# Kernel optimization log

Measured on AMD Instinct MI355X. Metric: run time of the kernel, lower is better.

Reference implementation:

```python
import jax, jax.numpy as jnp
import numpy as np

EPS = 1e-6
NHEAD = 12

def _ln(x):
    m = jnp.mean(x, -1, keepdims=True)
    v = jnp.var(x, -1, keepdims=True)
    return (x - m) * jax.lax.rsqrt(v + EPS)

def _modulate(x, shift, scale):
    return x * (1 + scale[:, None, :]) + shift[:, None, :]

def _pos_embedding(idx, dim, max_len=2048):
    K = jnp.arange(dim // 2)
    ang = idx[..., None] * jnp.pi / (max_len ** (2.0 * K / dim))
    return jnp.concatenate([jnp.sin(ang), jnp.cos(ang)], axis=-1)

def _forward(x, W_xemb, b_xemb, ds_table, sg_table, Wqkv, bqkv, Wo, bo, W1, b1, W2, b2,
             Wada, bada, Wada_f, bada_f, W_out, dataset, spacegroup, mask):
    B, N, _ = x.shape
    D = W_xemb.shape[1]
    hd = D // NHEAD
    # conditioning vector: label embeddings (eval mode: no cfg dropout)
    c = ds_table[dataset] + sg_table[spacegroup]                 # [B, D]
    h = x @ W_xemb + b_xemb + _pos_embedding(jnp.arange(N), D)[None]  # [B, N, D]
    kmask = mask[:, None, None, :]                                # [B,1,1,N], True = padded key
    scale_qk = 1.0 / jnp.sqrt(jnp.asarray(hd, h.dtype))

    def block(h, p):
        Wqkv, bqkv, Wo, bo, W1, b1, W2, b2, Wada, bada = p
        mods = jax.nn.silu(c) @ Wada + bada                      # [B, 6D]
        sh_a, sc_a, g_a, sh_m, sc_m, g_m = jnp.split(mods, 6, axis=-1)
        xm = _modulate(_ln(h), sh_a, sc_a)
        qkv = (xm @ Wqkv + bqkv).reshape(B, N, 3, NHEAD, hd)
        q, k, v = qkv[:, :, 0], qkv[:, :, 1], qkv[:, :, 2]
        scores = jnp.einsum('bqhd,bkhd->bhqk', q, k) * scale_qk   # MATH-backend path: full [B,H,N,N]
        scores = jnp.where(kmask, -jnp.inf, scores)
        attn = jax.nn.softmax(scores, axis=-1)
        o = jnp.einsum('bhqk,bkhd->bqhd', attn, v).reshape(B, N, D)
        o = o @ Wo + bo
        h = h + g_a[:, None, :] * o
        y = _modulate(_ln(h), sh_m, sc_m)
        y = jax.nn.gelu(y @ W1 + b1, approximate=True) @ W2 + b2
        h = h + g_m[:, None, :] * y
        return h, None

    h, _ = jax.lax.scan(block, h, (Wqkv, bqkv, Wo, bo, W1, b1, W2, b2, Wada, bada))
    mods_f = jax.nn.silu(c) @ Wada_f + bada_f
    sh_f, sc_f = jnp.split(mods_f, 2, axis=-1)
    return _modulate(_ln(h), sh_f, sc_f) @ W_out                  # [B, N, 1] per-token energy


def setup_inputs() -> dict:
    B, N, D, L, DX, HID = 32, 512, 768, 12, 8, 3072
    keys = iter(jax.random.split(jax.random.key(0), 32))
    def w(shape, s=0.02):
        return jax.random.normal(next(keys), shape, jnp.float32) * s
    return dict(
        x=jax.random.normal(next(keys), (B, N, 2 * DX), jnp.float32),
        W_xemb=w((2 * DX, D)), b_xemb=jnp.zeros((D,), jnp.float32),
        ds_table=w((3, D)), sg_table=w((231, D)),
        Wqkv=w((L, D, 3 * D)), bqkv=jnp.zeros((L, 3 * D), jnp.float32),
        Wo=w((L, D, D)), bo=jnp.zeros((L, D), jnp.float32),
        W1=w((L, D, HID)), b1=jnp.zeros((L, HID), jnp.float32),
        W2=w((L, HID, D)), b2=jnp.zeros((L, D), jnp.float32),
        Wada=w((L, D, 6 * D)), bada=jnp.zeros((L, 6 * D), jnp.float32),
        Wada_f=w((D, 2 * D)), bada_f=jnp.zeros((2 * D,), jnp.float32),
        W_out=w((D, 1)),
        dataset=jax.random.randint(next(keys), (32,), 0, 2),
        spacegroup=jax.random.randint(next(keys), (32,), 0, 230),
        mask=jax.random.bernoulli(next(keys), 0.1, (32, 512)),
    )


def reference(x, W_xemb, b_xemb, ds_table, sg_table, Wqkv, bqkv, Wo, bo, W1, b1, W2, b2,
              Wada, bada, Wada_f, bada_f, W_out, dataset, spacegroup, mask):
    return _forward(x, W_xemb, b_xemb, ds_table, sg_table, Wqkv, bqkv, Wo, bo, W1, b1,
                    W2, b2, Wada, bada, Wada_f, bada_f, W_out, dataset, spacegroup, mask)
```

## Files before the change

kernel.cpp:

```cpp
#include <hip/hip_runtime.h>
#include <hip/hip_bf16.h>

#define B_   32
#define N_   512
#define D_   768
#define H_   12
#define HID_ 3072
#define L_   12
#define M_   (B_*N_)

typedef __attribute__((ext_vector_type(8))) short short8_t;
typedef __attribute__((ext_vector_type(4))) short short4_t;
typedef __attribute__((ext_vector_type(4))) float f32x4;
typedef __hip_bfloat16 bf16;

__device__ __forceinline__ void gll16(const void* g, void* l){
    __builtin_amdgcn_global_load_lds((const __attribute__((address_space(1))) void*)g,
                                     (__attribute__((address_space(3))) void*)l, 16, 0, 0);
}

__global__ __launch_bounds__(256) void embed_kernel(
    const float* __restrict__ x, const float* __restrict__ Wx,
    const float* __restrict__ bx, float* __restrict__ h)
{
    long idx = (long)blockIdx.x * 256 + threadIdx.x;
    int d = (int)(idx % 768);
    long m = idx / 768;
    int n = (int)(m % 512);
    float acc = bx[d];
    const float* xr = x + m * 16;
    #pragma unroll
    for (int k = 0; k < 16; ++k) acc = fmaf(xr[k], Wx[k*768 + d], acc);
    int K = (d < 384) ? d : d - 384;
    float ang = (float)n * 3.14159265358979323846f * expf(-(2.0f*(float)K/768.0f) * 7.624618986159398f);
    acc += (d < 384) ? sinf(ang) : cosf(ang);
    h[idx] = acc;
}

__global__ __launch_bounds__(256) void csilu_kernel(
    const float* __restrict__ ds_t, const float* __restrict__ sg_t,
    const int* __restrict__ dataset, const int* __restrict__ sg, float* __restrict__ out)
{
    int idx = blockIdx.x*256 + threadIdx.x;
    int b = idx / 768, d = idx % 768;
    float c = ds_t[dataset[b]*768 + d] + sg_t[sg[b]*768 + d];
    out[idx] = c / (1.0f + expf(-c));
}

__global__ __launch_bounds__(256) void mods_part_kernel(
    const float* __restrict__ csilu, const float* __restrict__ W,
    float* __restrict__ part, int Nd2, long wLayerStride)
{
    __shared__ float cs[16][96];
    int n2 = blockIdx.x*256 + threadIdx.x;
    int l = blockIdx.y, z = blockIdx.z;
    int kz = z >> 1, bg = z & 1;
    int L = gridDim.y;
    for (int t = threadIdx.x; t < 16*96; t += 256){
        int bb = t / 96, kk = t - bb*96;
        cs[bb][kk] = csilu[(bg*16 + bb)*768 + kz*96 + kk];
    }
    __syncthreads();
    const float2* Wl = (const float2*)(W + (long)l*wLayerStride);
    float2 acc[16];
    #pragma unroll
    for (int b=0;b<16;b++) acc[b] = make_float2(0.f, 0.f);
    for (int k=0;k<96;++k){
        float2 wv = Wl[(long)(kz*96 + k)*Nd2 + n2];
        #pragma unroll
        for (int b=0;b<16;b++){
            float c = cs[b][k];
            acc[b].x = fmaf(c, wv.x, acc[b].x);
            acc[b].y = fmaf(c, wv.y, acc[b].y);
        }
    }
    float2* pp = (float2*)part + ((long)(kz*L + l)*32 + bg*16)*Nd2 + n2;
    #pragma unroll
    for (int b=0;b<16;b++) pp[(long)b*Nd2] = acc[b];
}

__global__ __launch_bounds__(256) void mods_reduce_kernel(
    const float* __restrict__ part, const float* __restrict__ bias,
    float* __restrict__ out, int Nd, int L)
{
    long idx = (long)blockIdx.x*256 + threadIdx.x;
    int n = (int)(idx % Nd);
    long r = idx / Nd;
    int b = (int)(r & 31);
    int l = (int)(r >> 5);
    float s = bias[(long)l*Nd + n];
    #pragma unroll
    for (int z=0;z<8;z++) s += part[((long)(z*L + l)*32 + b)*Nd + n];
    out[idx] = s;
}

__global__ __launch_bounds__(256) void transpose4_kernel(
    const float* __restrict__ Wqkv, const float* __restrict__ Wo,
    const float* __restrict__ W1,  const float* __restrict__ W2,
    bf16* __restrict__ wqT, bf16* __restrict__ woT,
    bf16* __restrict__ w1T, bf16* __restrict__ w2T)
{
    __shared__ float t[32][33];
    int tt = blockIdx.x;
    const float* src; bf16* dst; int K, Nd, nx;
    if (tt < 1728){ src=Wqkv; dst=wqT; K=768; Nd=2304; nx=72; }
    else if (tt < 2304){ src=Wo; dst=woT; K=768; Nd=768; nx=24; tt -= 1728; }
    else if (tt < 4608){ src=W1; dst=w1T; K=768; Nd=3072; nx=96; tt -= 2304; }
    else { src=W2; dst=w2T; K=3072; Nd=768; nx=24; tt -= 4608; }
    int n0 = (tt % nx)*32, k0 = (tt / nx)*32;
    int tx = threadIdx.x & 31, ty = threadIdx.x >> 5;
    #pragma unroll
    for (int j=0;j<4;j++)
        t[ty + j*8][tx] = src[(long)(k0 + ty + j*8)*Nd + n0 + tx];
    __syncthreads();
    #pragma unroll
    for (int j=0;j<4;j++)
        dst[(long)(n0 + ty + j*8)*K + k0 + tx] = __float2bfloat16(t[tx][ty + j*8]);
}

__global__ __launch_bounds__(256) void ln_mod_kernel(
    const float* __restrict__ h, const float* __restrict__ shiftB,
    const float* __restrict__ scaleB, int modsStride, bf16* __restrict__ out)
{
    int wave = threadIdx.x >> 6, lane = threadIdx.x & 63;
    long row = (long)blockIdx.x*4 + wave;
    int b = (int)(row >> 9);
    const float4* xr = (const float4*)(h + row*768);
    float4 v[3];
    float s = 0.f, ss = 0.f;
    #pragma unroll
    for (int i=0;i<3;i++){
        v[i] = xr[lane + i*64];
        s  += v[i].x + v[i].y + v[i].z + v[i].w;
        ss += v[i].x*v[i].x + v[i].y*v[i].y + v[i].z*v[i].z + v[i].w*v[i].w;
    }
    #pragma unroll
    for (int o=1;o<64;o<<=1){ s += __shfl_xor(s,o,64); ss += __shfl_xor(ss,o,64); }
    float mean = s * (1.0f/768.0f);
    float var  = ss * (1.0f/768.0f) - mean*mean;
    float rstd = rsqrtf(var + 1e-6f);
    const float4* sh4 = (const float4*)(shiftB + (long)b*modsStride);
    const float4* sc4 = (const float4*)(scaleB + (long)b*modsStride);
    short4_t* orow = (short4_t*)(out + row*768);
    #pragma unroll
    for (int i=0;i<3;i++){
        float4 sh = sh4[lane + i*64];
        float4 sc = sc4[lane + i*64];
        float o0 = (v[i].x-mean)*rstd*(1.f+sc.x) + sh.x;
        float o1 = (v[i].y-mean)*rstd*(1.f+sc.y) + sh.y;
        float o2 = (v[i].z-mean)*rstd*(1.f+sc.z) + sh.z;
        float o3 = (v[i].w-mean)*rstd*(1.f+sc.w) + sh.w;
        bf16 b0 = __float2bfloat16(o0), b1 = __float2bfloat16(o1);
        bf16 b2 = __float2bfloat16(o2), b3 = __float2bfloat16(o3);
        short4_t pk;
        pk[0] = *(short*)&b0; pk[1] = *(short*)&b1;
        pk[2] = *(short*)&b2; pk[3] = *(short*)&b3;
        orow[lane + i*64] = pk;
    }
}

__device__ __forceinline__ float gelu_f(float x){
    float z2 = 1.5957691216057308f * x * (1.0f + 0.044715f*x*x);
    return x / (1.0f + __expf(-z2));
}

template<int MODE>
__global__ __launch_bounds__(256, 2) void gemm128_kernel(
    const bf16* __restrict__ A, const bf16* __restrict__ Bw,
    const float* __restrict__ bias, bf16* __restrict__ outBf,
    float* __restrict__ hres, const float* __restrict__ gate,
    int Nd, int Kd, int gateStride)
{
    __shared__ __align__(16) short lds[40960];
    int tid = threadIdx.x;
    int lane = tid & 63, wave = tid >> 6;
    int frow = lane & 15, g = lane >> 4;

    int nx = gridDim.x;
    int bid = blockIdx.y * nx + blockIdx.x;
    int xcd = bid & 7;
    int wq  = bid >> 3;
    int mt  = xcd * 16 + (wq & 15);
    int ct  = wq >> 4;
    int m0 = mt * 128, n0 = ct * 192;
    int wn = wave * 48;

    const short* Ag = (const short*)A;
    const short* Bg = (const short*)Bw;
    int r0 = tid >> 3, s0 = (tid & 7) ^ ((tid >> 3) & 7);
    const short* aSrc = Ag + (long)(m0 + r0)*Kd + s0*8;
    const short* bSrc = Bg + (long)(n0 + r0)*Kd + s0*8;
    long rj = (long)32*Kd;
    int wbase = wave*512;

    int aFrag = frow*64;
    int bFrag = (wn + frow)*64;
    int slotK0 = (g ^ (frow & 7))*8;
    int slotK1 = ((4+g) ^ (frow & 7))*8;

    f32x4 acc[8][3];
    #pragma unroll
    for (int i=0;i<8;i++)
        #pragma unroll
        for (int j=0;j<3;j++) acc[i][j] = (f32x4){0.f,0.f,0.f,0.f};

    int NT = Kd >> 6;

#define STAGE(kt, ps) { \
    int par_ = (kt)&1; \
    if ((ps)==0){ \
        short* d_ = &lds[par_*8192 + wbase]; \
        gll16(aSrc +        (long)(kt)*64, d_); \
        gll16(aSrc +   rj + (long)(kt)*64, d_ + 2048); \
        gll16(aSrc + 2*rj + (long)(kt)*64, d_ + 4096); \
        gll16(aSrc + 3*rj + (long)(kt)*64, d_ + 6144); \
    } else { \
        short* d_ = &lds[16384 + par_*12288 + wbase]; \
        gll16(bSrc +        (long)(kt)*64, d_); \
        gll16(bSrc +   rj + (long)(kt)*64, d_ + 2048); \
        gll16(bSrc + 2*rj + (long)(kt)*64, d_ + 4096); \
        gll16(bSrc + 3*rj + (long)(kt)*64, d_ + 6144); \
        gll16(bSrc + 4*rj + (long)(kt)*64, d_ + 8192); \
        gll16(bSrc + 5*rj + (long)(kt)*64, d_ + 10240); \
    } }

    STAGE(0,0); STAGE(0,1);

    for (int kt=0; kt<NT; ++kt){
        int pA  = (kt&1)*8192;
        int pBb = 16384 + (kt&1)*12288;
        bool pf = (kt+1 < NT);
        if (pf){
            STAGE(kt+1, 0);
            asm volatile("s_waitcnt vmcnt(4)" ::: "memory");
        } else {
            asm volatile("s_waitcnt vmcnt(0)" ::: "memory");
        }
        __builtin_amdgcn_s_barrier();
        __builtin_amdgcn_sched_barrier(0);
        short8_t af[8], bfr[3];
        #pragma unroll
        for (int i=0;i<8;i++) af[i]  = *(const short8_t*)&lds[pA + aFrag + i*1024 + slotK0];
        #pragma unroll
        for (int j=0;j<3;j++) bfr[j] = *(const short8_t*)&lds[pBb + bFrag + j*1024 + slotK0];
        if (pf) STAGE(kt+1, 1);
        __builtin_amdgcn_s_setprio(1);
        #pragma unroll
        for (int i=0;i<8;i++)
            #pragma unroll
            for (int j=0;j<3;j++)
                acc[i][j] = __builtin_amdgcn_mfma_f32_16x16x32_bf16(af[i], bfr[j], acc[i][j], 0, 0, 0);
        __builtin_amdgcn_s_setprio(0);
        #pragma unroll
        for (int i=0;i<8;i++) af[i]  = *(const short8_t*)&lds[pA + aFrag + i*1024 + slotK1];
        #pragma unroll
        for (int j=0;j<3;j++) bfr[j] = *(const short8_t*)&lds[pBb + bFrag + j*1024 + slotK1];
        __builtin_amdgcn_s_setprio(1);
        #pragma unroll
        for (int i=0;i<8;i++)
            #pragma unroll
            for (int j=0;j<3;j++)
                acc[i][j] = __builtin_amdgcn_mfma_f32_16x16x32_bf16(af[i], bfr[j], acc[i][j], 0, 0, 0);
        __builtin_amdgcn_s_setprio(0);
        __builtin_amdgcn_sched_barrier(0);
        __builtin_amdgcn_s_barrier();
        __builtin_amdgcn_sched_barrier(0);
    }
#undef STAGE

    int rbase = m0 + g*4;
    int cbase = n0 + wn + frow;
    float bv0 = bias[cbase], bv1 = bias[cbase+16], bv2 = bias[cbase+32];
    #pragma unroll
    for (int i=0;i<8;i++){
        #pragma unroll
        for (int r=0;r<4;r++){
            int row = rbase + i*16 + r;
            float v0 = acc[i][0][r] + bv0;
            float v1 = acc[i][1][r] + bv1;
            float v2 = acc[i][2][r] + bv2;
            if (MODE == 0){
                bf16* o_ = outBf + (long)row*Nd + cbase;
                o_[0]  = __float2bfloat16(v0);
                o_[16] = __float2bfloat16(v1);
                o_[32] = __float2bfloat16(v2);
            } else if (MODE == 1){
                bf16* o_ = outBf + (long)row*Nd + cbase;
                o_[0]  = __float2bfloat16(gelu_f(v0));
                o_[16] = __float2bfloat16(gelu_f(v1));
                o_[32] = __float2bfloat16(gelu_f(v2));
            } else {
                int bb = row >> 9;
                const float* gp = gate + (long)bb*gateStride + cbase;
                float* hp = hres + (long)row*768 + cbase;
                hp[0]  += gp[0]  * v0;
                hp[16] += gp[16] * v1;
                hp[32] += gp[32] * v2;
            }
        }
    }
}

__global__ __launch_bounds__(256) void attn_mfma_kernel(
    const bf16* __restrict__ qkv, const int* __restrict__ mask, bf16* __restrict__ o)
{
    __shared__ __align__(16) short Ks[64][72];
    __shared__ __align__(16) short Vt[64][72];
    __shared__ __align__(16) short Ps[4][16][72];
    __shared__ float maskf[512];
    int tid = threadIdx.x, lane = tid & 63, wave = tid >> 6;
    int qt = blockIdx.x, hh = blockIdx.y, b = blockIdx.z;
    long base = (long)b * 512 * 2304;
    const short* qkvs = (const short*)qkv;

    maskf[tid]       = mask[b*512 + tid]       ? -1e30f : 0.0f;
    maskf[tid + 256] = mask[b*512 + tid + 256] ? -1e30f : 0.0f;

    int c = lane & 15, g = lane >> 4;
    int qrowA = qt*64 + wave*16 + c;
    const short* qptr = qkvs + base + (long)qrowA*2304 + hh*64 + g*8;
    short8_t qa0 = *(const short8_t*)qptr;
    short8_t qa1 = *(const short8_t*)(qptr + 32);

    f32x4 oacc[4];
    #pragma unroll
    for (int j=0;j<4;j++) oacc[j] = (f32x4){0.f,0.f,0.f,0.f};
    float m_r[4], l_r[4];
    #pragma unroll
    for (int r=0;r<4;r++){ m_r[r] = -50.0f; l_r[r] = 0.0f; }

    int kp = (tid & 31)*2, gv = tid >> 5;
    const short* kgbase = qkvs + base + 768  + hh*64;
    const short* vgbase = qkvs + base + 1536 + hh*64 + gv*8;

    for (int kt=0; kt<8; ++kt){
        __syncthreads();
        {
            int v0 = tid, v1 = tid + 256;
            int r0 = v0>>3, c0 = (v0&7)*8, r1 = v1>>3, c1 = (v1&7)*8;
            *(short8_t*)&Ks[r0][c0] = *(const short8_t*)(kgbase + (long)(kt*64 + r0)*2304 + c0);
            *(short8_t*)&Ks[r1][c1] = *(const short8_t*)(kgbase + (long)(kt*64 + r1)*2304 + c1);
            short8_t va = *(const short8_t*)(vgbase + (long)(kt*64 + kp    )*2304);
            short8_t vb = *(const short8_t*)(vgbase + (long)(kt*64 + kp + 1)*2304);
            #pragma unroll
            for (int e=0;e<8;e++){
                unsigned int pack = (unsigned int)(unsigned short)va[e]
                                  | ((unsigned int)(unsigned short)vb[e] << 16);
                *(unsigned int*)&Vt[gv*8 + e][kp] = pack;
            }
        }
        __syncthreads();
        f32x4 s[4];
        #pragma unroll
        for (int j=0;j<4;j++){
            short8_t kb0 = *(const short8_t*)&Ks[j*16 + c][g*8];
            short8_t kb1 = *(const short8_t*)&Ks[j*16 + c][g*8 + 32];
            f32x4 z = (f32x4){0.f,0.f,0.f,0.f};
            z = __builtin_amdgcn_mfma_f32_16x16x32_bf16(qa0, kb0, z, 0, 0, 0);
            z = __builtin_amdgcn_mfma_f32_16x16x32_bf16(qa1, kb1, z, 0, 0, 0);
            s[j] = z;
        }
        #pragma unroll
        for (int j=0;j<4;j++){
            float mbj = maskf[kt*64 + j*16 + c];
            #pragma unroll
            for (int r=0;r<4;r++) s[j][r] = s[j][r]*0.125f + mbj;
        }
        #pragma unroll
        for (int r=0;r<4;r++){
            float tm = fmaxf(fmaxf(s[0][r], s[1][r]), fmaxf(s[2][r], s[3][r]));
            #pragma unroll
            for (int o_=1;o_<16;o_<<=1) tm = fmaxf(tm, __shfl_xor(tm, o_, 64));
            float mn  = fmaxf(m_r[r], tm);
            float fac = __expf(m_r[r] - mn);
            m_r[r] = mn;
            float ls = l_r[r]*fac;
            #pragma unroll
            for (int j=0;j<4;j++){
                float p = __expf(s[j][r] - mn);
                s[j][r] = p;
                ls += p;
            }
            l_r[r] = ls;
            #pragma unroll
            for (int j=0;j<4;j++) oacc[j][r] *= fac;
        }
        #pragma unroll
        for (int j=0;j<4;j++)
            #pragma unroll
            for (int r=0;r<4;r++)
                *(bf16*)&Ps[wave][g*4 + r][j*16 + c] = __float2bfloat16(s[j][r]);
        short8_t pa0 = *(const short8_t*)&Ps[wave][c][g*8];
        short8_t pa1 = *(const short8_t*)&Ps[wave][c][g*8 + 32];
        #pragma unroll
        for (int j=0;j<4;j++){
            short8_t vb0 = *(const short8_t*)&Vt[j*16 + c][g*8];
            short8_t vb1 = *(const short8_t*)&Vt[j*16 + c][g*8 + 32];
            oacc[j] = __builtin_amdgcn_mfma_f32_16x16x32_bf16(pa0, vb0, oacc[j], 0, 0, 0);
            oacc[j] = __builtin_amdgcn_mfma_f32_16x16x32_bf16(pa1, vb1, oacc[j], 0, 0, 0);
        }
    }
    #pragma unroll
    for (int r=0;r<4;r++){
        float lt = l_r[r];
        #pragma unroll
        for (int o_=1;o_<16;o_<<=1) lt += __shfl_xor(lt, o_, 64);
        l_r[r] = 1.0f / lt;
    }
    int qrowC = qt*64 + wave*16 + g*4;
    bf16* orow = o + ((long)b*512 + qrowC)*768 + hh*64;
    #pragma unroll
    for (int r=0;r<4;r++)
        #pragma unroll
        for (int j=0;j<4;j++)
            orow[(long)r*768 + j*16 + c] = __float2bfloat16(oacc[j][r] * l_r[r]);
}

__global__ __launch_bounds__(256) void outdot_kernel(
    const bf16* __restrict__ xm, const float* __restrict__ Wout, float* __restrict__ out)
{
    int tid=threadIdx.x, lane=tid&63, wave=tid>>6;
    long row = (long)blockIdx.x*4 + wave;
    const bf16* xr = xm + row*768;
    float acc = 0.f;
    #pragma unroll
    for (int i=0;i<12;i++){ int d = lane + i*64; acc = fmaf(__bfloat162float(xr[d]), Wout[d], acc); }
    #pragma unroll
    for (int o_=1;o_<64;o_<<=1) acc += __shfl_xor(acc, o_, 64);
    if (lane==0) out[row] = acc;
}

extern "C" void kernel_launch(void* const* d_in, const int* in_sizes, int n_in,
                              void* d_out, int out_size, void* d_ws, size_t ws_size,
                              hipStream_t stream)
{
    const float* x      = (const float*)d_in[0];
    const float* W_xemb = (const float*)d_in[1];
    const float* b_xemb = (const float*)d_in[2];
    const float* ds_t   = (const float*)d_in[3];
    const float* sg_t   = (const float*)d_in[4];
    const float* Wqkv   = (const float*)d_in[5];
    const float* bqkv   = (const float*)d_in[6];
    const float* Wo     = (const float*)d_in[7];
    const float* bo     = (const float*)d_in[8];
    const float* W1     = (const float*)d_in[9];
    const float* b1     = (const float*)d_in[10];
    const float* W2     = (const float*)d_in[11];
    const float* b2     = (const float*)d_in[12];
    const float* Wada   = (const float*)d_in[13];
    const float* bada   = (const float*)d_in[14];
    const float* Wada_f = (const float*)d_in[15];
    const float* bada_f = (const float*)d_in[16];
    const float* W_out  = (const float*)d_in[17];
    const int* dataset  = (const int*)d_in[18];
    const int* sgroup   = (const int*)d_in[19];
    const int* mask     = (const int*)d_in[20];
    float* out = (float*)d_out;

    char* ws = (char*)d_ws;
    size_t off = 0;
    auto alloc = [&](size_t bytes)->void*{
        void* p = ws + off; off += (bytes + 255) & ~(size_t)255; return p; };
    float* h     = (float*)alloc((size_t)M_*768*4);
    float* csilu = (float*)alloc((size_t)32*768*4);
    float* modsA = (float*)alloc((size_t)12*32*4608*4);
    float* modsF = (float*)alloc((size_t)32*1536*4);
    bf16*  xm    = (bf16*) alloc((size_t)M_*768*2);
    bf16*  wbuf  = (bf16*) alloc((size_t)7077888*2);
    bf16*  big   = (bf16*) alloc((size_t)M_*3072*2);
    bf16* qkvb = big;
    bf16* y1   = big;
    float* partA = (float*)big;
    float* partF = partA + (size_t)8*12*32*4608;
    bf16* wqT = wbuf;
    bf16* woT = wqT + 2304*768;
    bf16* w1T = woT + 768*768;
    bf16* w2T = w1T + 3072*768;

    embed_kernel<<<49152, 256, 0, stream>>>(x, W_xemb, b_xemb, h);
    csilu_kernel<<<96, 256, 0, stream>>>(ds_t, sg_t, dataset, sgroup, csilu);
    mods_part_kernel<<<dim3(9,12,16), 256, 0, stream>>>(csilu, Wada, partA, 2304, (long)768*4608);
    mods_reduce_kernel<<<6912, 256, 0, stream>>>(partA, bada, modsA, 4608, 12);
    mods_part_kernel<<<dim3(3,1,16), 256, 0, stream>>>(csilu, Wada_f, partF, 768, 0);
    mods_reduce_kernel<<<192, 256, 0, stream>>>(partF, bada_f, modsF, 1536, 1);

    for (int l=0; l<12; ++l){
        const float* modsL = modsA + (long)l*32*4608;
        transpose4_kernel<<<6912, 256, 0, stream>>>(
            Wqkv + (long)l*768*2304, Wo + (long)l*768*768,
            W1 + (long)l*768*3072,  W2 + (long)l*3072*768,
            wqT, woT, w1T, w2T);

        ln_mod_kernel<<<4096, 256, 0, stream>>>(h, modsL + 0*768, modsL + 1*768, 4608, xm);
        gemm128_kernel<0><<<dim3(12, 128), 256, 0, stream>>>(xm, wqT, bqkv + l*2304, qkvb,
                                                             nullptr, nullptr, 2304, 768, 0);
        attn_mfma_kernel<<<dim3(8, 12, 32), 256, 0, stream>>>(qkvb, mask, xm);
        gemm128_kernel<2><<<dim3(4, 128), 256, 0, stream>>>(xm, woT, bo + l*768, nullptr,
                                                            h, modsL + 2*768, 768, 768, 4608);
        ln_mod_kernel<<<4096, 256, 0, stream>>>(h, modsL + 3*768, modsL + 4*768, 4608, xm);
        gemm128_kernel<1><<<dim3(16, 128), 256, 0, stream>>>(xm, w1T, b1 + l*3072, y1,
                                                             nullptr, nullptr, 3072, 768, 0);
        gemm128_kernel<2><<<dim3(4, 128), 256, 0, stream>>>(y1, w2T, b2 + l*768, nullptr,
                                                            h, modsL + 5*768, 768, 3072, 4608);
    }
    ln_mod_kernel<<<4096, 256, 0, stream>>>(h, modsF + 0, modsF + 768, 1536, xm);
    outdot_kernel<<<4096, 256, 0, stream>>>(xm, W_out, out);
}
```

Measured before the change: 4.749 ms.

## Replace 128x192 GEMM tiles with 256x256 eight-wave ping-pong pipelined kernel

After: 5.346 ms. +12.6%, slower.

```diff
diff --git a/kernel.cpp b/kernel.cpp
--- a/kernel.cpp
+++ b/kernel.cpp
@@ -165,137 +165,177 @@
 }
 
 template<int MODE>
-__global__ __launch_bounds__(256, 2) void gemm128_kernel(
+__global__ __launch_bounds__(512, 2) void gemm256_kernel(
     const bf16* __restrict__ A, const bf16* __restrict__ Bw,
     const float* __restrict__ bias, bf16* __restrict__ outBf,
     float* __restrict__ hres, const float* __restrict__ gate,
     int Nd, int Kd, int gateStride)
 {
-    __shared__ __align__(16) short lds[40960];
+    __shared__ __align__(16) short lds[65536];
     int tid = threadIdx.x;
     int lane = tid & 63, wave = tid >> 6;
     int frow = lane & 15, g = lane >> 4;
-
-    int nx = gridDim.x;
-    int bid = blockIdx.y * nx + blockIdx.x;
-    int xcd = bid & 7;
-    int wq  = bid >> 3;
-    int mt  = xcd * 16 + (wq & 15);
-    int ct  = wq >> 4;
-    int m0 = mt * 128, n0 = ct * 192;
-    int wn = wave * 48;
+    int wm = wave >> 2, wn4 = wave & 3;
+
+    int nwg = gridDim.x;
+    int bid = blockIdx.x;
+    int q8  = nwg >> 3;
+    int wgid = (bid & 7) * q8 + (bid >> 3);
+    int ntiles = Nd >> 8;
+    int mt = wgid / ntiles, ct = wgid - mt*ntiles;
+    int m0 = mt * 256, n0 = ct * 256;
 
     const short* Ag = (const short*)A;
     const short* Bg = (const short*)Bw;
-    int r0 = tid >> 3, s0 = (tid & 7) ^ ((tid >> 3) & 7);
+    int r0 = tid >> 3;
+    int s0 = (tid & 7) ^ (r0 & 7);
     const short* aSrc = Ag + (long)(m0 + r0)*Kd + s0*8;
     const short* bSrc = Bg + (long)(n0 + r0)*Kd + s0*8;
-    long rj = (long)32*Kd;
-    int wbase = wave*512;
-
-    int aFrag = frow*64;
-    int bFrag = (wn + frow)*64;
+    long r64 = (long)64*Kd;
+    int wb = wave*512;
+
+    int aRd = wm*4096 + frow*64;
+    int bRd = wn4*2048 + frow*64;
     int slotK0 = (g ^ (frow & 7))*8;
     int slotK1 = ((4+g) ^ (frow & 7))*8;
 
-    f32x4 acc[8][3];
+    f32x4 acc[8][4];
     #pragma unroll
     for (int i=0;i<8;i++)
         #pragma unroll
-        for (int j=0;j<3;j++) acc[i][j] = (f32x4){0.f,0.f,0.f,0.f};
+        for (int j=0;j<4;j++) acc[i][j] = (f32x4){0.f,0.f,0.f,0.f};
+
+    short8_t af[4][2];
+    short8_t bf[2][2];
 
     int NT = Kd >> 6;
 
-#define STAGE(kt, ps) { \
-    int par_ = (kt)&1; \
-    if ((ps)==0){ \
-        short* d_ = &lds[par_*8192 + wbase]; \
-        gll16(aSrc +        (long)(kt)*64, d_); \
-        gll16(aSrc +   rj + (long)(kt)*64, d_ + 2048); \
-        gll16(aSrc + 2*rj + (long)(kt)*64, d_ + 4096); \
-        gll16(aSrc + 3*rj + (long)(kt)*64, d_ + 6144); \
-    } else { \
-        short* d_ = &lds[16384 + par_*12288 + wbase]; \
-        gll16(bSrc +        (long)(kt)*64, d_); \
-        gll16(bSrc +   rj + (long)(kt)*64, d_ + 2048); \
-        gll16(bSrc + 2*rj + (long)(kt)*64, d_ + 4096); \
-        gll16(bSrc + 3*rj + (long)(kt)*64, d_ + 6144); \
-        gll16(bSrc + 4*rj + (long)(kt)*64, d_ + 8192); \
-        gll16(bSrc + 5*rj + (long)(kt)*64, d_ + 10240); \
-    } }
-
-    STAGE(0,0); STAGE(0,1);
+#define STA(kt, h) { \
+    short* d_ = &lds[((kt)&1)*16384 + (h)*8192 + wb]; \
+    const short* s_ = aSrc + (long)(h)*2*r64 + (long)(kt)*64; \
+    gll16(s_, d_); gll16(s_ + r64, d_ + 4096); }
+#define STB(kt, h) { \
+    short* d_ = &lds[32768 + ((kt)&1)*16384 + (h)*8192 + wb]; \
+    const short* s_ = bSrc + (long)(h)*2*r64 + (long)(kt)*64; \
+    gll16(s_, d_); gll16(s_ + r64, d_ + 4096); }
+
+#define RDA(mh) { \
+    int ba_ = pA + (mh)*8192 + aRd; \
+    _Pragma("unroll") \
+    for (int i=0;i<4;++i){ \
+        af[i][0] = *(const short8_t*)&lds[ba_ + i*1024 + slotK0]; \
+        af[i][1] = *(const short8_t*)&lds[ba_ + i*1024 + slotK1]; } }
+#define RDB(nh) { \
+    int bb_ = pB + (nh)*8192 + bRd; \
+    _Pragma("unroll") \
+    for (int j=0;j<2;++j){ \
+        bf[j][0] = *(const short8_t*)&lds[bb_ + j*1024 + slotK0]; \
+        bf[j][1] = *(const short8_t*)&lds[bb_ + j*1024 + slotK1]; } }
+
+#define MFMA16(mh, nh) { \
+    __builtin_amdgcn_s_setprio(1); \
+    _Pragma("unroll") \
+    for (int kh=0;kh<2;++kh) \
+        _Pragma("unroll") \
+        for (int i=0;i<4;++i) \
+            _Pragma("unroll") \
+            for (int j=0;j<2;++j) \
+                acc[(mh)*4+i][(nh)*2+j] = __builtin_amdgcn_mfma_f32_16x16x32_bf16( \
+                    af[i][kh], bf[j][kh], acc[(mh)*4+i][(nh)*2+j], 0, 0, 0); \
+    __builtin_amdgcn_s_setprio(0); }
+
+    STA(0,0); STB(0,0); STB(0,1); STA(0,1);
+    asm volatile("s_waitcnt vmcnt(4)" ::: "memory");
+    __builtin_amdgcn_s_barrier();
+    __builtin_amdgcn_sched_barrier(0);
 
     for (int kt=0; kt<NT; ++kt){
-        int pA  = (kt&1)*8192;
-        int pBb = 16384 + (kt&1)*12288;
+        int pA = (kt&1)*16384;
+        int pB = 32768 + (kt&1)*16384;
         bool pf = (kt+1 < NT);
-        if (pf){
-            STAGE(kt+1, 0);
-            asm volatile("s_waitcnt vmcnt(4)" ::: "memory");
-        } else {
-            asm volatile("s_waitcnt vmcnt(0)" ::: "memory");
-        }
-        __builtin_amdgcn_s_barrier();
-        __builtin_amdgcn_sched_barrier(0);
-        short8_t af[8], bfr[3];
-        #pragma unroll
-        for (int i=0;i<8;i++) af[i]  = *(const short8_t*)&lds[pA + aFrag + i*1024 + slotK0];
-        #pragma unroll
-        for (int j=0;j<3;j++) bfr[j] = *(const short8_t*)&lds[pBb + bFrag + j*1024 + slotK0];
-        if (pf) STAGE(kt+1, 1);
-        __builtin_amdgcn_s_setprio(1);
-        #pragma unroll
-        for (int i=0;i<8;i++)
-            #pragma unroll
-            for (int j=0;j<3;j++)
-                acc[i][j] = __builtin_amdgcn_mfma_f32_16x16x32_bf16(af[i], bfr[j], acc[i][j], 0, 0, 0);
-        __builtin_amdgcn_s_setprio(0);
-        #pragma unroll
-        for (int i=0;i<8;i++) af[i]  = *(const short8_t*)&lds[pA + aFrag + i*1024 + slotK1];
-        #pragma unroll
-        for (int j=0;j<3;j++) bfr[j] = *(const short8_t*)&lds[pBb + bFrag + j*1024 + slotK1];
-        __builtin_amdgcn_s_setprio(1);
-        #pragma unroll
-        for (int i=0;i<8;i++)
-            #pragma unroll
-            for (int j=0;j<3;j++)
-                acc[i][j] = __builtin_amdgcn_mfma_f32_16x16x32_bf16(af[i], bfr[j], acc[i][j], 0, 0, 0);
-        __builtin_amdgcn_s_setprio(0);
-        __builtin_amdgcn_sched_barrier(0);
-        __builtin_amdgcn_s_barrier();
-        __builtin_amdgcn_sched_barrier(0);
-    }
-#undef STAGE
-
-    int rbase = m0 + g*4;
-    int cbase = n0 + wn + frow;
-    float bv0 = bias[cbase], bv1 = bias[cbase+16], bv2 = bias[cbase+32];
-    #pragma unroll
-    for (int i=0;i<8;i++){
-        #pragma unroll
-        for (int r=0;r<4;r++){
-            int row = rbase + i*16 + r;
-            float v0 = acc[i][0][r] + bv0;
-            float v1 = acc[i][1][r] + bv1;
-            float v2 = acc[i][2][r] + bv2;
-            if (MODE == 0){
-                bf16* o_ = outBf + (long)row*Nd + cbase;
-                o_[0]  = __float2bfloat16(v0);
-                o_[16] = __float2bfloat16(v1);
-                o_[32] = __float2bfloat16(v2);
-            } else if (MODE == 1){
-                bf16* o_ = outBf + (long)row*Nd + cbase;
-                o_[0]  = __float2bfloat16(gelu_f(v0));
-                o_[16] = __float2bfloat16(gelu_f(v1));
-                o_[32] = __float2bfloat16(gelu_f(v2));
-            } else {
-                int bb = row >> 9;
-                const float* gp = gate + (long)bb*gateStride + cbase;
-                float* hp = hres + (long)row*768 + cbase;
-                hp[0]  += gp[0]  * v0;
-                hp[16] += gp[16] * v1;
-                hp[32] += gp[32] * v2;
+
+        RDA(0); RDB(0);
+        if (pf) STA(kt+1, 0);
+        __builtin_amdgcn_s_barrier();
+        __builtin_amdgcn_sched_barrier(0);
+        MFMA16(0, 0);
+        __builtin_amdgcn_sched_barrier(0);
+        if (pf) asm volatile("s_waitcnt vmcnt(4)" ::: "memory");
+        else    asm volatile("s_waitcnt vmcnt(2)" ::: "memory");
+        __builtin_amdgcn_s_barrier();
+        __builtin_amdgcn_sched_barrier(0);
+
+        RDB(1);
+        if (pf) STB(kt+1, 0);
+        __builtin_amdgcn_s_barrier();
+        __builtin_amdgcn_sched_barrier(0);
+        MFMA16(0, 1);
+        __builtin_amdgcn_sched_barrier(0);
+        if (pf) asm volatile("s_waitcnt vmcnt(4)" ::: "memory");
+        else    asm volatile("s_waitcnt vmcnt(0)" ::: "memory");
+        __builtin_amdgcn_s_barrier();
+        __builtin_amdgcn_sched_barrier(0);
+
+        RDA(1);
+        if (pf) STB(kt+1, 1);
+        __builtin_amdgcn_s_barrier();
+        __builtin_amdgcn_sched_barrier(0);
+        MFMA16(1, 1);
+        __builtin_amdgcn_sched_barrier(0);
+        __builtin_amdgcn_s_barrier();
+        __builtin_amdgcn_sched_barrier(0);
+
+        RDB(0);
+        if (pf) STA(kt+1, 1);
+        __builtin_amdgcn_s_barrier();
+        __builtin_amdgcn_sched_barrier(0);
+        MFMA16(1, 0);
+        __builtin_amdgcn_sched_barrier(0);
+        if (pf) asm volatile("s_waitcnt vmcnt(4)" ::: "memory");
+        __builtin_amdgcn_s_barrier();
+        __builtin_amdgcn_sched_barrier(0);
+    }
+#undef STA
+#undef STB
+#undef RDA
+#undef RDB
+#undef MFMA16
+
+    int rb = m0 + wm*64 + g*4;
+    int cb = n0 + wn4*32 + frow;
+    float bv0 = bias[cb], bv1 = bias[cb+16], bv2 = bias[cb+128], bv3 = bias[cb+144];
+    #pragma unroll
+    for (int mh=0; mh<2; ++mh){
+        #pragma unroll
+        for (int i=0;i<4;++i){
+            #pragma unroll
+            for (int r=0;r<4;++r){
+                int row = rb + mh*128 + i*16 + r;
+                float v0 = acc[mh*4+i][0][r] + bv0;
+                float v1 = acc[mh*4+i][1][r] + bv1;
+                float v2 = acc[mh*4+i][2][r] + bv2;
+                float v3 = acc[mh*4+i][3][r] + bv3;
+                if (MODE == 0){
+                    bf16* o_ = outBf + (long)row*Nd + cb;
+                    o_[0]   = __float2bfloat16(v0);
+                    o_[16]  = __float2bfloat16(v1);
+                    o_[128] = __float2bfloat16(v2);
+                    o_[144] = __float2bfloat16(v3);
+                } else if (MODE == 1){
+                    bf16* o_ = outBf + (long)row*Nd + cb;
+                    o_[0]   = __float2bfloat16(gelu_f(v0));
+                    o_[16]  = __float2bfloat16(gelu_f(v1));
+                    o_[128] = __float2bfloat16(gelu_f(v2));
+                    o_[144] = __float2bfloat16(gelu_f(v3));
+                } else {
+                    int bb = row >> 9;
+                    const float* gp = gate + (long)bb*gateStride + cb;
+                    float* hp = hres + (long)row*768 + cb;
+                    hp[0]   += gp[0]   * v0;
+                    hp[16]  += gp[16]  * v1;
+                    hp[128] += gp[128] * v2;
+                    hp[144] += gp[144] * v3;
+                }
             }
         }
     }
@@ -492,16 +532,16 @@
             wqT, woT, w1T, w2T);
 
         ln_mod_kernel<<<4096, 256, 0, stream>>>(h, modsL + 0*768, modsL + 1*768, 4608, xm);
-        gemm128_kernel<0><<<dim3(12, 128), 256, 0, stream>>>(xm, wqT, bqkv + l*2304, qkvb,
-                                                             nullptr, nullptr, 2304, 768, 0);
+        gemm256_kernel<0><<<576, 512, 0, stream>>>(xm, wqT, bqkv + l*2304, qkvb,
+                                                   nullptr, nullptr, 2304, 768, 0);
         attn_mfma_kernel<<<dim3(8, 12, 32), 256, 0, stream>>>(qkvb, mask, xm);
-        gemm128_kernel<2><<<dim3(4, 128), 256, 0, stream>>>(xm, woT, bo + l*768, nullptr,
-                                                            h, modsL + 2*768, 768, 768, 4608);
+        gemm256_kernel<2><<<192, 512, 0, stream>>>(xm, woT, bo + l*768, nullptr,
+                                                   h, modsL + 2*768, 768, 768, 4608);
         ln_mod_kernel<<<4096, 256, 0, stream>>>(h, modsL + 3*768, modsL + 4*768, 4608, xm);
-        gemm128_kernel<1><<<dim3(16, 128), 256, 0, stream>>>(xm, w1T, b1 + l*3072, y1,
-                                                             nullptr, nullptr, 3072, 768, 0);
-        gemm128_kernel<2><<<dim3(4, 128), 256, 0, stream>>>(y1, w2T, b2 + l*768, nullptr,
-                                                            h, modsL + 5*768, 768, 3072, 4608);
+        gemm256_kernel<1><<<768, 512, 0, stream>>>(xm, w1T, b1 + l*3072, y1,
+                                                   nullptr, nullptr, 3072, 768, 0);
+        gemm256_kernel<2><<<192, 512, 0, stream>>>(y1, w2T, b2 + l*768, nullptr,
+                                                   h, modsL + 5*768, 768, 3072, 4608);
     }
     ln_mod_kernel<<<4096, 256, 0, stream>>>(h, modsF + 0, modsF + 768, 1536, xm);
     outdot_kernel<<<4096, 256, 0, stream>>>(xm, W_out, out);
```
